# Kernel tuning notes

Measured on AMD Instinct MI355X. Metric: run time of the kernel, lower is better.

The kernel has to match this reference:

```python
import jax, jax.numpy as jnp
import numpy as np

BATCH, SEQ, D_IN, D_STATE = 8, 4096, 1024, 64


def setup_inputs() -> dict:
    key = jax.random.key(0)
    ks = jax.random.split(key, 3)
    u = jax.random.normal(ks[0], (BATCH, SEQ, D_IN), dtype=jnp.float32)
    log_A = jnp.zeros((D_STATE,), dtype=jnp.float32)
    B = jax.random.normal(ks[1], (D_STATE, D_IN), dtype=jnp.float32) * 0.01
    C = jax.random.normal(ks[2], (D_IN, D_STATE), dtype=jnp.float32) * 0.01
    D = jnp.ones((D_IN,), dtype=jnp.float32)
    log_delta = jnp.zeros((D_IN,), dtype=jnp.float32)
    return {"u": u, "log_A": log_A, "B": B, "C": C, "D": D, "log_delta": log_delta}


def reference(u, log_A, B, C, D, log_delta):
    batch, seq_len, input_dim = u.shape
    state_dim = log_A.shape[0]
    delta = jax.nn.softplus(log_delta)                      # [I]
    A = -jnp.exp(log_A)                                     # [N]
    A_bar = jnp.exp(delta[:, None] * A[None, :])            # [I, N]
    A_bar_state = A_bar.mean(axis=0)                        # [N]
    B_bar = B * delta[None, :]                              # [N, I]
    # Precompute input projections for all timesteps: [B, T, N]
    Bu = jnp.einsum('ni,bti->btn', B_bar, u)
    x0 = jnp.zeros((batch, state_dim), dtype=u.dtype)

    def step(x, bu_t):
        x = x * A_bar_state[None, :] + bu_t
        return x, x

    _, xs = jax.lax.scan(step, x0, jnp.swapaxes(Bu, 0, 1))  # xs: [T, B, N]
    xs = jnp.swapaxes(xs, 0, 1)                             # [B, T, N]
    y = jnp.einsum('in,btn->bti', C, xs) + D[None, None, :] * u
    return y
```

## Files before the change

### kernel.cpp

```cpp
#include <hip/hip_runtime.h>
#include <cstdint>

#define BATCH 8
#define SEQ   4096
#define DIN   1024
#define DST   64
#define CHUNK 32
#define NCC   (SEQ/CHUNK)
#define NBLK1 (BATCH*NCC)

typedef __attribute__((ext_vector_type(8))) short short8;
typedef __attribute__((ext_vector_type(4))) short short4v;
typedef __attribute__((ext_vector_type(4))) float f32x4;

__device__ __forceinline__ short f2bf(float f) {
    union { float f; unsigned u; } v; v.f = f;
    unsigned r = v.u + 0x7fffu + ((v.u >> 16) & 1u);
    return (short)(r >> 16);
}
__device__ __forceinline__ float softplus_f(float x) {
    return (x > 20.f) ? x : log1pf(expf(x));
}

__global__ void ssm_k0(const float* __restrict__ logA, const float* __restrict__ Bm,
                       const float* __restrict__ Cm, const float* __restrict__ logdelta,
                       short* __restrict__ Bb, short* __restrict__ Cb,
                       float* __restrict__ a_o, float* __restrict__ l2a_o,
                       float* __restrict__ aL_o)
{
    __shared__ float red[256];
    int blk = blockIdx.x, tid = threadIdx.x;
    if (blk < DST) {
        int n = blk;
        float An = -expf(logA[n]);
        float acc = 0.f;
        #pragma unroll
        for (int ii = 0; ii < DIN/256; ++ii) {
            int i = ii*256 + tid;
            float dlt = softplus_f(logdelta[i]);
            Bb[n*DIN + i] = f2bf(Bm[n*DIN + i] * dlt);
            acc += expf(dlt * An);
        }
        red[tid] = acc; __syncthreads();
        for (int s = 128; s > 0; s >>= 1) {
            if (tid < s) red[tid] += red[tid + s];
            __syncthreads();
        }
        if (tid == 0) {
            float a = red[0] * (1.f/DIN);
            a_o[n]   = a;
            l2a_o[n] = log2f(a);
            float p = a;
            #pragma unroll
            for (int q = 0; q < 5; ++q) p = p*p;
            aL_o[n] = p;
        }
    } else {
        int base = (blk - DST) * (DIN*DST/16);
        for (int e = tid; e < DIN*DST/16; e += 256)
            Cb[base + e] = f2bf(Cm[base + e]);
    }
}

__global__ __launch_bounds__(256) void ssm_k1(
    const float* __restrict__ u, const short* __restrict__ Bb,
    const float* __restrict__ a_i, float* __restrict__ xloc, float* __restrict__ carry)
{
    int blk = blockIdx.x;
    int b = blk >> 7, cc = blk & (NCC-1);
    int tid = threadIdx.x;
    int w = tid >> 6, lane = tid & 63;
    int wr = w & 1, wk = w >> 1;
    int m = lane & 15, quad = lane >> 4;

    long row = ((long)b << 12) + (cc << 5) + (wr << 4) + m;
    const float* up  = u  + row * DIN + wk*(DIN/2) + quad * 8;
    const short* bb0 = Bb + wk*(DIN/2) + quad * 8;

    f32x4 acc0 = {0,0,0,0}, acc1 = {0,0,0,0}, acc2 = {0,0,0,0}, acc3 = {0,0,0,0};

    #pragma unroll 4
    for (int ks = 0; ks < DIN/64; ++ks) {
        const float4* uv = (const float4*)(up + ks*32);
        float4 ua = uv[0];
        float4 ub = uv[1];
        short8 af;
        af[0]=f2bf(ua.x); af[1]=f2bf(ua.y); af[2]=f2bf(ua.z); af[3]=f2bf(ua.w);
        af[4]=f2bf(ub.x); af[5]=f2bf(ub.y); af[6]=f2bf(ub.z); af[7]=f2bf(ub.w);
        const short* bbase = bb0 + ks*32;
        short8 b0 = *(const short8*)(bbase + ( 0 + m)*DIN);
        short8 b1 = *(const short8*)(bbase + (16 + m)*DIN);
        short8 b2 = *(const short8*)(bbase + (32 + m)*DIN);
        short8 b3 = *(const short8*)(bbase + (48 + m)*DIN);
        acc0 = __builtin_amdgcn_mfma_f32_16x16x32_bf16(af, b0, acc0, 0,0,0);
        acc1 = __builtin_amdgcn_mfma_f32_16x16x32_bf16(af, b1, acc1, 0,0,0);
        acc2 = __builtin_amdgcn_mfma_f32_16x16x32_bf16(af, b2, acc2, 0,0,0);
        acc3 = __builtin_amdgcn_mfma_f32_16x16x32_bf16(af, b3, acc3, 0,0,0);
    }

    __shared__ float bu[2][CHUNK][DST+4];
    int trow = (wr << 4) + (quad << 2);
    #pragma unroll
    for (int r = 0; r < 4; ++r) {
        bu[wk][trow + r][ 0 + m] = acc0[r];
        bu[wk][trow + r][16 + m] = acc1[r];
        bu[wk][trow + r][32 + m] = acc2[r];
        bu[wk][trow + r][48 + m] = acc3[r];
    }
    __syncthreads();

    if (tid < DST) {
        int n = tid;
        float an = a_i[n];
        float x = 0.f;
        float* xp = xloc + (((long)b << 12) + (cc << 5)) * DST + n;
        #pragma unroll
        for (int t = 0; t < CHUNK; ++t) {
            x = x * an + (bu[0][t][n] + bu[1][t][n]);
            xp[(long)t * DST] = x;
        }
        carry[blk * DST + n] = x;
    }
}

__global__ __launch_bounds__(256) void ssm_k3(
    const float* __restrict__ u, const float* __restrict__ xloc,
    const float* __restrict__ carry, const float* __restrict__ aLp,
    const float* __restrict__ l2a, const short* __restrict__ Cb,
    const float* __restrict__ Dv, float* __restrict__ y)
{
    int tblk = blockIdx.x;
    long t0 = (long)tblk << 4;
    int b = (int)(t0 >> 12);
    int tloc0 = (int)(t0 & (SEQ-1));
    int c = tloc0 >> 5;
    int jbase = tloc0 & (CHUNK-1);

    __shared__ float E_lds[DST];
    __shared__ short xs[16][72];
    __shared__ float ybuf[16][260];

    int tid = threadIdx.x;
    if (tid < DST) {
        int n = tid;
        float al = aLp[n];
        float E = 0.f;
        const float* cp = carry + (b*NCC)*DST + n;
        for (int p = 0; p < c; ++p)
            E = E * al + cp[p*DST];
        E_lds[n] = E;
    }
    __syncthreads();

    {
        int m  = tid >> 4;
        int n0 = (tid & 15) * 4;
        long t = t0 + m;
        int j  = jbase + m;
        float4 xv = *(const float4*)(xloc + t*DST + n0);
        float4 la = *(const float4*)(l2a + n0);
        float4 Ev = *(const float4*)(&E_lds[n0]);
        float jp = (float)(j + 1);
        short4v xsv;
        xsv[0] = f2bf(xv.x + exp2f(jp*la.x)*Ev.x);
        xsv[1] = f2bf(xv.y + exp2f(jp*la.y)*Ev.y);
        xsv[2] = f2bf(xv.z + exp2f(jp*la.z)*Ev.z);
        xsv[3] = f2bf(xv.w + exp2f(jp*la.w)*Ev.w);
        *(short4v*)(&xs[m][n0]) = xsv;
    }
    __syncthreads();

    int w = tid >> 6, lane = tid & 63;
    int l16 = lane & 15, quad = lane >> 4;

    short8 x0 = *(const short8*)(&xs[l16][ 0 + quad*8]);
    short8 x1 = *(const short8*)(&xs[l16][32 + quad*8]);

    for (int s = 0; s < 4; ++s) {
        #pragma unroll
        for (int ii = 0; ii < 4; ++ii) {
            int i0 = s*256 + w*64 + ii*16;
            const short* cb = Cb + (long)(i0 + l16)*DST + quad*8;
            short8 c0 = *(const short8*)(cb);
            short8 c1 = *(const short8*)(cb + 32);
            f32x4 acc = {0,0,0,0};
            acc = __builtin_amdgcn_mfma_f32_16x16x32_bf16(c0, x0, acc, 0,0,0);
            acc = __builtin_amdgcn_mfma_f32_16x16x32_bf16(c1, x1, acc, 0,0,0);
            *(f32x4*)(&ybuf[l16][w*64 + ii*16 + (quad << 2)]) = acc;
        }
        __syncthreads();
        #pragma unroll
        for (int k = 0; k < 4; ++k) {
            int f4 = k*256 + tid;
            int row = f4 >> 6, c4 = f4 & 63;
            int col = c4 * 4;
            int gcol = s*256 + col;
            long t = t0 + row;
            f32x4 yv = *(const f32x4*)(&ybuf[row][col]);
            const f32x4 uu = *(const f32x4*)(u + t*DIN + gcol);
            const f32x4 dd = *(const f32x4*)(Dv + gcol);
            f32x4 o;
            o.x = yv.x + dd.x*uu.x;
            o.y = yv.y + dd.y*uu.y;
            o.z = yv.z + dd.z*uu.z;
            o.w = yv.w + dd.w*uu.w;
            __builtin_nontemporal_store(o, (f32x4*)(y + t*DIN + gcol));
        }
        __syncthreads();
    }
}

extern "C" void kernel_launch(void* const* d_in, const int* in_sizes, int n_in,
                              void* d_out, int out_size, void* d_ws, size_t ws_size,
                              hipStream_t stream)
{
    const float* u        = (const float*)d_in[0];
    const float* logA     = (const float*)d_in[1];
    const float* Bm       = (const float*)d_in[2];
    const float* Cm       = (const float*)d_in[3];
    const float* D        = (const float*)d_in[4];
    const float* logdelta = (const float*)d_in[5];
    float* y = (float*)d_out;

    char* ws = (char*)d_ws;
    float* xloc  = (float*)(ws);
    float* carry = (float*)(ws + 8u*1024*1024);
    short* Bb    = (short*)(ws + 8u*1024*1024 + 256*1024);
    short* Cb    = (short*)(ws + 8u*1024*1024 + 384*1024);
    float* a_o   = (float*)(ws + 8u*1024*1024 + 512*1024);
    float* l2a_o = a_o + 64;
    float* aL_o  = a_o + 128;

    hipLaunchKernelGGL(ssm_k0, dim3(DST + 16), dim3(256), 0, stream,
                       logA, Bm, Cm, logdelta, Bb, Cb, a_o, l2a_o, aL_o);
    hipLaunchKernelGGL(ssm_k1, dim3(NBLK1), dim3(256), 0, stream,
                       u, Bb, a_o, xloc, carry);
    hipLaunchKernelGGL(ssm_k3, dim3((BATCH*SEQ)/16), dim3(256), 0, stream,
                       u, xloc, carry, aL_o, l2a_o, Cb, D, y);
}
```

Baseline: 316.7 us.

## Add parallel carry-scan kernel to replace per-block serial chunk prefix

Adds a new kernel that runs a Hillis-Steele scan over chunk carries per batch in shared memory and writes each chunk's incoming state. ssm_k3 then loads that state directly, instead of every block serially folding up to 127 carries. The change also raises the unroll factor in the projection loop and replaces the nontemporal output store with a normal store. The cost is one extra small kernel launch with only 8 blocks, plus extra workspace.

```diff
diff --git a/kernel.cpp b/kernel.cpp
--- a/kernel.cpp
+++ b/kernel.cpp
@@ -79,7 +79,7 @@
 
     f32x4 acc0 = {0,0,0,0}, acc1 = {0,0,0,0}, acc2 = {0,0,0,0}, acc3 = {0,0,0,0};
 
-    #pragma unroll 4
+    #pragma unroll 8
     for (int ks = 0; ks < DIN/64; ++ks) {
         const float4* uv = (const float4*)(up + ks*32);
         float4 ua = uv[0];
@@ -113,21 +113,53 @@
         int n = tid;
         float an = a_i[n];
         float x = 0.f;
-        float* xp = xloc + (((long)b << 12) + (cc << 5)) * DST + n;
         #pragma unroll
         for (int t = 0; t < CHUNK; ++t) {
             x = x * an + (bu[0][t][n] + bu[1][t][n]);
-            xp[(long)t * DST] = x;
+            xp_store:
+            xloc[(((long)b << 12) + (cc << 5) + t) * DST + n] = x;
         }
         carry[blk * DST + n] = x;
+    }
+}
+
+__global__ __launch_bounds__(256) void ssm_k2(
+    const float* __restrict__ carry, const float* __restrict__ aLp,
+    float* __restrict__ Xin)
+{
+    __shared__ float v[2][NCC][DST+1];
+    int b = blockIdx.x, tid = threadIdx.x;
+    int n = tid & 63;
+    for (int f = tid; f < NCC*DST; f += 256) {
+        int c = f >> 6, nn = f & 63;
+        v[0][c][nn] = carry[(b*NCC + c)*DST + nn];
+    }
+    float fd = aLp[n];
+    __syncthreads();
+    int pp = 0;
+    for (int d = 1; d < NCC; d <<= 1) {
+        #pragma unroll 4
+        for (int r = 0; r < NCC/4; ++r) {
+            int c = (tid >> 6) + r*4;
+            float val = v[pp][c][n];
+            if (c >= d) val += fd * v[pp][c-d][n];
+            v[pp^1][c][n] = val;
+        }
+        fd *= fd;
+        pp ^= 1;
+        __syncthreads();
+    }
+    for (int f = tid; f < NCC*DST; f += 256) {
+        int c = f >> 6, nn = f & 63;
+        Xin[(b*NCC + c)*DST + nn] = (c == 0) ? 0.f : v[pp][c-1][nn];
     }
 }
 
 __global__ __launch_bounds__(256) void ssm_k3(
     const float* __restrict__ u, const float* __restrict__ xloc,
-    const float* __restrict__ carry, const float* __restrict__ aLp,
-    const float* __restrict__ l2a, const short* __restrict__ Cb,
-    const float* __restrict__ Dv, float* __restrict__ y)
+    const float* __restrict__ Xin, const float* __restrict__ l2a,
+    const short* __restrict__ Cb, const float* __restrict__ Dv,
+    float* __restrict__ y)
 {
     int tblk = blockIdx.x;
     long t0 = (long)tblk << 4;
@@ -141,15 +173,8 @@
     __shared__ float ybuf[16][260];
 
     int tid = threadIdx.x;
-    if (tid < DST) {
-        int n = tid;
-        float al = aLp[n];
-        float E = 0.f;
-        const float* cp = carry + (b*NCC)*DST + n;
-        for (int p = 0; p < c; ++p)
-            E = E * al + cp[p*DST];
-        E_lds[n] = E;
-    }
+    if (tid < DST)
+        E_lds[tid] = Xin[(b*NCC + c)*DST + tid];
     __syncthreads();
 
     {
@@ -204,7 +229,7 @@
             o.y = yv.y + dd.y*uu.y;
             o.z = yv.z + dd.z*uu.z;
             o.w = yv.w + dd.w*uu.w;
-            __builtin_nontemporal_store(o, (f32x4*)(y + t*DIN + gcol));
+            *(f32x4*)(y + t*DIN + gcol) = o;
         }
         __syncthreads();
     }
@@ -225,9 +250,10 @@
     char* ws = (char*)d_ws;
     float* xloc  = (float*)(ws);
     float* carry = (float*)(ws + 8u*1024*1024);
-    short* Bb    = (short*)(ws + 8u*1024*1024 + 256*1024);
-    short* Cb    = (short*)(ws + 8u*1024*1024 + 384*1024);
-    float* a_o   = (float*)(ws + 8u*1024*1024 + 512*1024);
+    float* Xin   = (float*)(ws + 8u*1024*1024 + 256*1024);
+    short* Bb    = (short*)(ws + 8u*1024*1024 + 512*1024);
+    short* Cb    = (short*)(ws + 8u*1024*1024 + 640*1024);
+    float* a_o   = (float*)(ws + 8u*1024*1024 + 768*1024);
     float* l2a_o = a_o + 64;
     float* aL_o  = a_o + 128;
 
@@ -235,6 +261,8 @@
                        logA, Bm, Cm, logdelta, Bb, Cb, a_o, l2a_o, aL_o);
     hipLaunchKernelGGL(ssm_k1, dim3(NBLK1), dim3(256), 0, stream,
                        u, Bb, a_o, xloc, carry);
+    hipLaunchKernelGGL(ssm_k2, dim3(BATCH), dim3(256), 0, stream,
+                       carry, aL_o, Xin);
     hipLaunchKernelGGL(ssm_k3, dim3((BATCH*SEQ)/16), dim3(256), 0, stream,
-                       u, xloc, carry, aL_o, l2a_o, Cb, D, y);
-}
+                       u, xloc, Xin, l2a_o, Cb, D, y);
+}
```

After: 309.3 us. -2.3%, faster.
